# Performance work log

Measured on AMD Instinct MI355X. Metric: run time of the kernel, lower is better.

The kernel has to match this reference:

```python
import jax, jax.numpy as jnp
import numpy as np

TOP_K = 6
N_EXPERTS = 64
N_GROUP = 8
TOPK_GROUP = 3
HIDDEN = 4096
BATCH, SEQ = 4, 4096


def setup_inputs() -> dict:
    key = jax.random.key(0)
    k1, k2 = jax.random.split(key)
    x = jax.random.normal(k1, (BATCH, SEQ, HIDDEN), dtype=jnp.float32)
    # kaiming_uniform_(a=sqrt(5)) on (E, H) -> U(-1/sqrt(H), 1/sqrt(H))
    bound = 1.0 / np.sqrt(HIDDEN)
    weight = jax.random.uniform(k2, (N_EXPERTS, HIDDEN), minval=-bound, maxval=bound, dtype=jnp.float32)
    return {"x": x, "weight": weight}


def reference(x, weight):
    # Flatten tokens: (B, S, H) -> (T, H)
    T = x.shape[0] * x.shape[1]
    h = x.reshape(T, HIDDEN).astype(jnp.float32)
    # Router logits and probabilities, fp32 as in the original.
    logits = jnp.einsum('th,eh->te', h, weight.astype(jnp.float32))  # (T, E)
    scores = jax.nn.softmax(logits, axis=-1)
    # Group-limited greedy: pick topk_group groups by per-group max score.
    epg = N_EXPERTS // N_GROUP
    group_max = scores.reshape(T, N_GROUP, epg).max(axis=-1)          # (T, G)
    _, gidx = jax.lax.top_k(group_max, TOPK_GROUP)                    # (T, Kg)
    group_mask = jax.nn.one_hot(gidx, N_GROUP, dtype=scores.dtype).sum(axis=1)  # (T, G)
    expert_mask = jnp.repeat(group_mask, epg, axis=-1)                # (T, E)
    masked_scores = jnp.where(expert_mask > 0, scores, 0.0)
    # Final top-k over masked scores. torch used sorted=False; jax returns
    # sorted descending -- same expert set and weights, order may differ.
    topk_weight, topk_idx = jax.lax.top_k(masked_scores, TOP_K)      # (T, k)
    return topk_idx, topk_weight
```

## Files before the change

### kernel.cpp

```cpp
#include <hip/hip_runtime.h>
#include <hip/hip_bf16.h>


#define TM     32
#define HK     128
#define PITCH  132
#define NE     64
#define NH     4096
#define NTOPK  6

__global__ __launch_bounds__(256, 2) void moe_gate_kernel(
    const float* __restrict__ x, const float* __restrict__ w,
    float* __restrict__ out_idx, float* __restrict__ out_w)
{
    __shared__ float xs[TM * PITCH];
    __shared__ float ws[NE * PITCH];

    const int tid = threadIdx.x;
    const int tx  = tid & 15;
    const int ty  = tid >> 4;
    const int t0  = blockIdx.x * TM;

    float acc[2][4];
    #pragma unroll
    for (int i = 0; i < 2; ++i)
        #pragma unroll
        for (int j = 0; j < 4; ++j) acc[i][j] = 0.f;

    const int c4 = (tid & 31) << 2;
    const int r0 = tid >> 5;

    for (int k0 = 0; k0 < NH; k0 += HK) {
        #pragma unroll
        for (int p = 0; p < 4; ++p) {
            const int r = r0 + (p << 3);
            const float4 v = *reinterpret_cast<const float4*>(
                x + (size_t)(t0 + r) * NH + k0 + c4);
            *reinterpret_cast<float4*>(&xs[r * PITCH + c4]) = v;
        }
        #pragma unroll
        for (int p = 0; p < 8; ++p) {
            const int r = r0 + (p << 3);
            const float4 v = *reinterpret_cast<const float4*>(
                w + (size_t)r * NH + k0 + c4);
            *reinterpret_cast<float4*>(&ws[r * PITCH + c4]) = v;
        }
        __syncthreads();

        #pragma unroll 8
        for (int kk = 0; kk < HK; kk += 4) {
            const float4 xa = *reinterpret_cast<const float4*>(&xs[ty * PITCH + kk]);
            const float4 xb = *reinterpret_cast<const float4*>(&xs[(ty + 16) * PITCH + kk]);
            #pragma unroll
            for (int j = 0; j < 4; ++j) {
                const float4 wv = *reinterpret_cast<const float4*>(
                    &ws[(tx + (j << 4)) * PITCH + kk]);
                acc[0][j] = fmaf(xa.x, wv.x, acc[0][j]);
                acc[0][j] = fmaf(xa.y, wv.y, acc[0][j]);
                acc[0][j] = fmaf(xa.z, wv.z, acc[0][j]);
                acc[0][j] = fmaf(xa.w, wv.w, acc[0][j]);
                acc[1][j] = fmaf(xb.x, wv.x, acc[1][j]);
                acc[1][j] = fmaf(xb.y, wv.y, acc[1][j]);
                acc[1][j] = fmaf(xb.z, wv.z, acc[1][j]);
                acc[1][j] = fmaf(xb.w, wv.w, acc[1][j]);
            }
        }
        __syncthreads();
    }

    float* lg = ws;
    #pragma unroll
    for (int i = 0; i < 2; ++i)
        #pragma unroll
        for (int j = 0; j < 4; ++j)
            lg[(ty + (i << 4)) * 66 + (tx + (j << 4))] = acc[i][j];
    __syncthreads();

    const int lane = tid & 63;
    const int wid  = tid >> 6;
    for (int tt = wid * 8; tt < wid * 8 + 8; ++tt) {
        const float logit = lg[tt * 66 + lane];

        float m = logit;
        #pragma unroll
        for (int s = 32; s > 0; s >>= 1) m = fmaxf(m, __shfl_xor(m, s));
        const float ex = expf(logit - m);
        float sum = ex;
        #pragma unroll
        for (int s = 32; s > 0; s >>= 1) sum += __shfl_xor(sum, s);
        const float score = ex / sum;

        float gm = score;
        #pragma unroll
        for (int s = 4; s > 0; s >>= 1) gm = fmaxf(gm, __shfl_xor(gm, s));
        const int g = lane >> 3;

        int grank = 0;
        #pragma unroll
        for (int gg = 0; gg < 8; ++gg) {
            const float o = __shfl(gm, gg << 3);
            grank += (o > gm) || (o == gm && gg < g);
        }
        const float masked = (grank < 3) ? score : 0.0f;

        int rank = 0;
        for (int ee = 0; ee < 64; ++ee) {
            const float o = __shfl(masked, ee);
            rank += (o > masked) || (o == masked && ee < lane);
        }
        if (rank < NTOPK) {
            const int t = t0 + tt;
            out_idx[t * NTOPK + rank] = (float)lane;
            out_w[t * NTOPK + rank]   = masked;
        }
    }
}

extern "C" void kernel_launch(void* const* d_in, const int* in_sizes, int n_in,
                              void* d_out, int out_size, void* d_ws, size_t ws_size,
                              hipStream_t stream) {
    const float* x = (const float*)d_in[0];
    const float* w = (const float*)d_in[1];
    const int T = in_sizes[0] / NH;
    float* outf    = (float*)d_out;
    float* out_idx = outf;
    float* out_w   = outf + (size_t)T * NTOPK;

    dim3 grid(T / TM), block(256);
    hipLaunchKernelGGL(moe_gate_kernel, grid, block, 0, stream,
                       x, w, out_idx, out_w);
}
```

Baseline: 485.3 us.

## Split-K GEMM into separate kernel with larger token tile, then gate kernel

Splits the router GEMM into two K halves across blocks and doubles the token tile to 64, giving each thread a 4x4 register tile for more FMA per shared-memory load. Partial logits go to a workspace, and a second kernel sums the halves and runs softmax with group-limited top-k. The block count stays the same while per-block work on x doubles and W reloads per token drop. It adds a global round trip for partials and a second launch.

```diff
diff --git a/kernel.cpp b/kernel.cpp
--- a/kernel.cpp
+++ b/kernel.cpp
@@ -2,84 +2,103 @@
 #include <hip/hip_bf16.h>
 
 
-#define TM     32
+#define TM     64
 #define HK     128
 #define PITCH  132
 #define NE     64
 #define NH     4096
+#define KSPLIT 2
+#define KHALF  (NH / KSPLIT)
 #define NTOPK  6
 
-__global__ __launch_bounds__(256, 2) void moe_gate_kernel(
+__global__ __launch_bounds__(256, 2) void moe_gemm_kernel(
     const float* __restrict__ x, const float* __restrict__ w,
-    float* __restrict__ out_idx, float* __restrict__ out_w)
+    float* __restrict__ partial, int T)
 {
     __shared__ float xs[TM * PITCH];
     __shared__ float ws[NE * PITCH];
 
-    const int tid = threadIdx.x;
-    const int tx  = tid & 15;
-    const int ty  = tid >> 4;
-    const int t0  = blockIdx.x * TM;
+    const int tid  = threadIdx.x;
+    const int tx   = tid & 15;
+    const int ty   = tid >> 4;
+    const int blk  = blockIdx.x;
+    const int t0   = (blk >> 1) * TM;
+    const int kb   = (blk & 1) * KHALF;
 
-    float acc[2][4];
+    float acc[4][4];
     #pragma unroll
-    for (int i = 0; i < 2; ++i)
+    for (int i = 0; i < 4; ++i)
         #pragma unroll
         for (int j = 0; j < 4; ++j) acc[i][j] = 0.f;
 
     const int c4 = (tid & 31) << 2;
     const int r0 = tid >> 5;
 
-    for (int k0 = 0; k0 < NH; k0 += HK) {
+    const float* xrow = xs + ty * PITCH;
+    const float* wrow = ws + tx * PITCH;
+
+    for (int k0 = 0; k0 < KHALF; k0 += HK) {
         #pragma unroll
-        for (int p = 0; p < 4; ++p) {
+        for (int p = 0; p < 8; ++p) {
             const int r = r0 + (p << 3);
             const float4 v = *reinterpret_cast<const float4*>(
-                x + (size_t)(t0 + r) * NH + k0 + c4);
+                x + (size_t)(t0 + r) * NH + kb + k0 + c4);
             *reinterpret_cast<float4*>(&xs[r * PITCH + c4]) = v;
         }
         #pragma unroll
         for (int p = 0; p < 8; ++p) {
             const int r = r0 + (p << 3);
             const float4 v = *reinterpret_cast<const float4*>(
-                w + (size_t)r * NH + k0 + c4);
+                w + (size_t)r * NH + kb + k0 + c4);
             *reinterpret_cast<float4*>(&ws[r * PITCH + c4]) = v;
         }
         __syncthreads();
 
         #pragma unroll 8
         for (int kk = 0; kk < HK; kk += 4) {
-            const float4 xa = *reinterpret_cast<const float4*>(&xs[ty * PITCH + kk]);
-            const float4 xb = *reinterpret_cast<const float4*>(&xs[(ty + 16) * PITCH + kk]);
+            float4 xa[4], wv[4];
+            xa[0] = *reinterpret_cast<const float4*>(xrow + kk);
+            xa[1] = *reinterpret_cast<const float4*>(xrow + 16 * PITCH + kk);
+            xa[2] = *reinterpret_cast<const float4*>(xrow + 32 * PITCH + kk);
+            xa[3] = *reinterpret_cast<const float4*>(xrow + 48 * PITCH + kk);
+            wv[0] = *reinterpret_cast<const float4*>(wrow + kk);
+            wv[1] = *reinterpret_cast<const float4*>(wrow + 16 * PITCH + kk);
+            wv[2] = *reinterpret_cast<const float4*>(wrow + 32 * PITCH + kk);
+            wv[3] = *reinterpret_cast<const float4*>(wrow + 48 * PITCH + kk);
             #pragma unroll
-            for (int j = 0; j < 4; ++j) {
-                const float4 wv = *reinterpret_cast<const float4*>(
-                    &ws[(tx + (j << 4)) * PITCH + kk]);
-                acc[0][j] = fmaf(xa.x, wv.x, acc[0][j]);
-                acc[0][j] = fmaf(xa.y, wv.y, acc[0][j]);
-                acc[0][j] = fmaf(xa.z, wv.z, acc[0][j]);
-                acc[0][j] = fmaf(xa.w, wv.w, acc[0][j]);
-                acc[1][j] = fmaf(xb.x, wv.x, acc[1][j]);
-                acc[1][j] = fmaf(xb.y, wv.y, acc[1][j]);
-                acc[1][j] = fmaf(xb.z, wv.z, acc[1][j]);
-                acc[1][j] = fmaf(xb.w, wv.w, acc[1][j]);
-            }
+            for (int i = 0; i < 4; ++i)
+                #pragma unroll
+                for (int j = 0; j < 4; ++j) {
+                    acc[i][j] = fmaf(xa[i].x, wv[j].x, acc[i][j]);
+                    acc[i][j] = fmaf(xa[i].y, wv[j].y, acc[i][j]);
+                    acc[i][j] = fmaf(xa[i].z, wv[j].z, acc[i][j]);
+                    acc[i][j] = fmaf(xa[i].w, wv[j].w, acc[i][j]);
+                }
         }
         __syncthreads();
     }
 
-    float* lg = ws;
+    float* pbase = partial + (size_t)(blk & 1) * T * NE;
     #pragma unroll
-    for (int i = 0; i < 2; ++i)
+    for (int i = 0; i < 4; ++i)
         #pragma unroll
         for (int j = 0; j < 4; ++j)
-            lg[(ty + (i << 4)) * 66 + (tx + (j << 4))] = acc[i][j];
-    __syncthreads();
+            pbase[(size_t)(t0 + ty + (i << 4)) * NE + tx + (j << 4)] = acc[i][j];
+}
 
+__global__ __launch_bounds__(256, 4) void moe_gate_kernel(
+    const float* __restrict__ partial,
+    float* __restrict__ out_idx, float* __restrict__ out_w, int T)
+{
+    const int tid  = threadIdx.x;
     const int lane = tid & 63;
     const int wid  = tid >> 6;
-    for (int tt = wid * 8; tt < wid * 8 + 8; ++tt) {
-        const float logit = lg[tt * 66 + lane];
+    const int tb   = blockIdx.x * 32 + wid * 8;
+
+    for (int tt = 0; tt < 8; ++tt) {
+        const int t = tb + tt;
+        const float logit = partial[(size_t)t * NE + lane]
+                          + partial[(size_t)(T + t) * NE + lane];
 
         float m = logit;
         #pragma unroll
@@ -109,7 +128,6 @@
             rank += (o > masked) || (o == masked && ee < lane);
         }
         if (rank < NTOPK) {
-            const int t = t0 + tt;
             out_idx[t * NTOPK + rank] = (float)lane;
             out_w[t * NTOPK + rank]   = masked;
         }
@@ -125,8 +143,12 @@
     float* outf    = (float*)d_out;
     float* out_idx = outf;
     float* out_w   = outf + (size_t)T * NTOPK;
+    float* partial = (float*)d_ws;
 
-    dim3 grid(T / TM), block(256);
-    hipLaunchKernelGGL(moe_gate_kernel, grid, block, 0, stream,
-                       x, w, out_idx, out_w);
+    dim3 gg((T / TM) * KSPLIT), gb(256);
+    hipLaunchKernelGGL(moe_gemm_kernel, gg, gb, 0, stream, x, w, partial, T);
+
+    dim3 hg(T / 32), hb(256);
+    hipLaunchKernelGGL(moe_gate_kernel, hg, hb, 0, stream,
+                       partial, out_idx, out_w, T);
 }
```

Measured after the change: 447.4 us. -7.8%, faster.
